# Optimization experiments

Measured on AMD Instinct MI355X. Metric: run time of the kernel, lower is better.

The kernel has to match this reference:

```python
import math
import jax, jax.numpy as jnp
import numpy as np

D_MODEL = 256
N_HEADS = 8
D_K = D_MODEL // N_HEADS
BS = 2
SEQ = 2048
NEG = -1e32


def _linear(x, W, b):
    return x @ W + b


def _layernorm(x, g, b):
    m = jnp.mean(x, axis=-1, keepdims=True)
    v = jnp.mean((x - m) ** 2, axis=-1, keepdims=True)
    return (x - m) / jnp.sqrt(v + 1e-5) * g + b


def _attention(q, k, v, mask, gammas):
    # q,k,v: [b,h,s,dk]; mask: [1,1,s,s] bool; gammas: [h,1,1]
    d_k = q.shape[-1]
    scores = jnp.einsum('bhqd,bhkd->bhqk', q, k) / math.sqrt(d_k)
    S = scores.shape[-1]
    # distance-decay bias (computed under stop_gradient, as torch.no_grad + detach)
    sm = jax.lax.stop_gradient(jax.nn.softmax(jnp.where(mask, scores, NEG), axis=-1))
    distcum = jnp.cumsum(sm, axis=-1)
    disttot = jnp.sum(sm, axis=-1, keepdims=True)
    idx = jnp.arange(S, dtype=scores.dtype)
    pos = jnp.abs(idx[None, :] - idx[:, None])[None, None]  # |i-j|
    dist = jax.lax.stop_gradient(
        jnp.sqrt(jnp.clip((disttot - distcum) * pos, 0.0, None)))
    gamma = -jax.nn.softplus(gammas)[None]  # [1,h,1,1]
    eff = jnp.clip(jnp.exp(dist * gamma), 1e-5, 1e5)
    scores = jnp.where(mask, scores * eff, NEG)
    scores = jnp.where(mask, jax.nn.softmax(scores, axis=-1), 0.0)
    return jnp.einsum('bhqk,bhkd->bhqd', scores, v)


def _mha(qx, kx, vx, Wq, bq, Wk, bk, Wv, bv, Wo, bo, gammas, mask):
    bs = qx.shape[0]
    def split(x, W, b):
        return _linear(x, W, b).reshape(bs, -1, N_HEADS, D_K).transpose(0, 2, 1, 3)
    q = split(qx, Wq, bq)
    k = split(kx, Wk, bk)
    v = split(vx, Wv, bv)
    o = _attention(q, k, v, mask, gammas)
    o = o.transpose(0, 2, 1, 3).reshape(bs, -1, D_MODEL)
    return _linear(o, Wo, bo)


def _layer(query, key, values, Wq, bq, Wk, bk, Wv, bv, Wo, bo, gammas, ln_g, ln_b, peek_cur):
    S = query.shape[1]
    mask = jnp.tril(jnp.ones((S, S), dtype=bool), 0 if peek_cur else -1)[None, None]
    out = _mha(query, key, values, Wq, bq, Wk, bk, Wv, bv, Wo, bo, gammas, mask)
    return _layernorm(query + out, ln_g, ln_b)


def _forward(q_emb, qa_emb,
             b1_Wq, b1_bq, b1_Wv, b1_bv, b1_Wo, b1_bo, b1_gam, b1_lng, b1_lnb,
             b2_Wq, b2_bq, b2_Wv, b2_bv, b2_Wo, b2_bo, b2_gam, b2_lng, b2_lnb,
             b3_Wq, b3_bq, b3_Wk, b3_bk, b3_Wv, b3_bv, b3_Wo, b3_bo, b3_gam, b3_lng, b3_lnb,
             know_params, lk_W, lk_b, lv_W, lv_b):
    # blocks 1 & 2: kq_same -> k projection shares q projection weights
    hq = _layer(q_emb, q_emb, q_emb,
                b1_Wq, b1_bq, b1_Wq, b1_bq, b1_Wv, b1_bv, b1_Wo, b1_bo,
                b1_gam, b1_lng, b1_lnb, peek_cur=True)
    ha = _layer(qa_emb, qa_emb, qa_emb,
                b2_Wq, b2_bq, b2_Wq, b2_bq, b2_Wv, b2_bv, b2_Wo, b2_bo,
                b2_gam, b2_lng, b2_lnb, peek_cur=True)
    query = jnp.broadcast_to(know_params, hq.shape)
    h = _layer(query, hq, ha,
               b3_Wq, b3_bq, b3_Wk, b3_bk, b3_Wv, b3_bv, b3_Wo, b3_bo,
               b3_gam, b3_lng, b3_lnb, peek_cur=False)
    bs, S, d = hq.shape
    key = jax.nn.sigmoid(_linear(
        jnp.broadcast_to(know_params, (bs, S, d)).reshape(bs, S, N_HEADS, D_K),
        lk_W, lk_b)).reshape(bs * S, N_HEADS, d)
    value = jax.nn.sigmoid(_linear(
        h.reshape(bs, S, N_HEADS, D_K), lv_W, lv_b)).reshape(bs * S, N_HEADS, d)
    beta = jnp.einsum('nhd,nd->nh', key, q_emb.reshape(bs * S, d))
    alpha = jax.nn.softmax(beta, axis=-1)
    h = jnp.einsum('nh,nhd->nd', alpha, value).reshape(bs, S, d)
    return h


def setup_inputs() -> dict:
    keys = iter(jax.random.split(jax.random.key(0), 64))
    def nrm(shape, scale=0.02):
        return jax.random.normal(next(keys), shape, dtype=jnp.float32) * scale
    def uni(shape):
        return jax.random.uniform(next(keys), shape, dtype=jnp.float32, minval=-1.0, maxval=1.0)
    d = D_MODEL
    inp = {
        'q_emb': nrm((BS, SEQ, d), 1.0),
        'qa_emb': nrm((BS, SEQ, d), 1.0),
    }
    for blk in ('b1', 'b2'):
        inp[blk + '_Wq'] = nrm((d, d)); inp[blk + '_bq'] = jnp.zeros((d,), jnp.float32)
        inp[blk + '_Wv'] = nrm((d, d)); inp[blk + '_bv'] = jnp.zeros((d,), jnp.float32)
        inp[blk + '_Wo'] = nrm((d, d)); inp[blk + '_bo'] = jnp.zeros((d,), jnp.float32)
        inp[blk + '_gam'] = uni((N_HEADS, 1, 1))
        inp[blk + '_lng'] = jnp.ones((d,), jnp.float32)
        inp[blk + '_lnb'] = jnp.zeros((d,), jnp.float32)
    inp['b3_Wq'] = nrm((d, d)); inp['b3_bq'] = jnp.zeros((d,), jnp.float32)
    inp['b3_Wk'] = nrm((d, d)); inp['b3_bk'] = jnp.zeros((d,), jnp.float32)
    inp['b3_Wv'] = nrm((d, d)); inp['b3_bv'] = jnp.zeros((d,), jnp.float32)
    inp['b3_Wo'] = nrm((d, d)); inp['b3_bo'] = jnp.zeros((d,), jnp.float32)
    inp['b3_gam'] = uni((N_HEADS, 1, 1))
    inp['b3_lng'] = jnp.ones((d,), jnp.float32)
    inp['b3_lnb'] = jnp.zeros((d,), jnp.float32)
    inp['know_params'] = uni((1, 1, d))
    inp['lk_W'] = nrm((D_K, d)); inp['lk_b'] = jnp.zeros((d,), jnp.float32)
    inp['lv_W'] = nrm((D_K, d)); inp['lv_b'] = jnp.zeros((d,), jnp.float32)
    return inp


def reference(q_emb, qa_emb,
              b1_Wq, b1_bq, b1_Wv, b1_bv, b1_Wo, b1_bo, b1_gam, b1_lng, b1_lnb,
              b2_Wq, b2_bq, b2_Wv, b2_bv, b2_Wo, b2_bo, b2_gam, b2_lng, b2_lnb,
              b3_Wq, b3_bq, b3_Wk, b3_bk, b3_Wv, b3_bv, b3_Wo, b3_bo, b3_gam, b3_lng, b3_lnb,
              know_params, lk_W, lk_b, lv_W, lv_b):
    return _forward(q_emb, qa_emb,
                    b1_Wq, b1_bq, b1_Wv, b1_bv, b1_Wo, b1_bo, b1_gam, b1_lng, b1_lnb,
                    b2_Wq, b2_bq, b2_Wv, b2_bv, b2_Wo, b2_bo, b2_gam, b2_lng, b2_lnb,
                    b3_Wq, b3_bq, b3_Wk, b3_bk, b3_Wv, b3_bv, b3_Wo, b3_bo, b3_gam, b3_lng, b3_lnb,
                    know_params, lk_W, lk_b, lv_W, lv_b)
```

## Files before the change

kernel.cpp:

```cpp
#include <hip/hip_runtime.h>
#include <hip/hip_bf16.h>

#define DM 256
#define NH 8
#define DK 32
#define BSZ 2
#define SEQ 2048
#define ROWS (BSZ*SEQ)
#define RT 16
#define SRB 2312

static __device__ __forceinline__ int sw8(int j) { return j + ((j >> 6) << 3); }

typedef __attribute__((ext_vector_type(8))) short short8;
typedef __attribute__((ext_vector_type(4))) float f32x4;

static __device__ __forceinline__ unsigned short f2bf(float f) {
    unsigned u = __float_as_uint(f);
    return (unsigned short)((u + 0x7FFFu + ((u >> 16) & 1u)) >> 16);
}
static __device__ __forceinline__ float bf2f(unsigned short h) {
    return __uint_as_float(((unsigned)h) << 16);
}

static __device__ __forceinline__ unsigned cvtpk(float lo, float hi) {
    unsigned r;
    asm("v_cvt_pk_bf16_f32 %0, %1, %2" : "=v"(r) : "v"(lo), "v"(hi));
    return r;
}

static __device__ __forceinline__ float ex2(float x) { return __builtin_amdgcn_exp2f(x); }
static __device__ __forceinline__ float sqt(float x) { return __builtin_amdgcn_sqrtf(x); }
static __device__ __forceinline__ float rcp(float x) { return __builtin_amdgcn_rcpf(x); }

template<int CTRL, int RM>
static __device__ __forceinline__ float dppadd(float x) {
    int s = __builtin_amdgcn_update_dpp(0, __float_as_int(x), CTRL, RM, 0xf, true);
    return x + __int_as_float(s);
}
static __device__ __forceinline__ float scan32(float x) {
    x = dppadd<0x111, 0xf>(x);
    x = dppadd<0x112, 0xf>(x);
    x = dppadd<0x114, 0xf>(x);
    x = dppadd<0x118, 0xf>(x);
    x = dppadd<0x142, 0xa>(x);
    return x;
}
static __device__ __forceinline__ float red16(float x) {
    x = dppadd<0x0B1, 0xf>(x);
    x = dppadd<0x04E, 0xf>(x);
    x = dppadd<0x124, 0xf>(x);
    x = dppadd<0x128, 0xf>(x);
    return x;
}
static __device__ __forceinline__ float bcast31(float x) {
    return __int_as_float(__builtin_amdgcn_ds_swizzle(__float_as_int(x), 0x03E0));
}
static __device__ __forceinline__ float swz_x16(float x) {
    return __int_as_float(__builtin_amdgcn_ds_swizzle(__float_as_int(x), 0x401F));
}

static __device__ __forceinline__ void unpack4(uint2 u, float& s0, float& s1,
                                               float& s2, float& s3) {
    s0 = __uint_as_float(u.x << 16);
    s1 = __uint_as_float(u.x & 0xFFFF0000u);
    s2 = __uint_as_float(u.y << 16);
    s3 = __uint_as_float(u.y & 0xFFFF0000u);
}

static __device__ __forceinline__ uint2 decay_quad(
    float s0, float s1, float s2, float s3v,
    float e0, float e1, float e2, float e3,
    float cum, float pq, float linv,
    float l, float gamma2, float& l2)
{
    float p0, p1, p2, p3;
    cum += e0;
    { float dist = sqt(fmaxf((l - cum) * pq, 0.f));
      float eff = fmaxf(ex2(dist * gamma2), 1e-5f);
      p0 = ex2(s0 * eff); l2 += p0; }
    cum += e1;
    { float dist = sqt(fmaxf((l - cum) * (pq - linv), 0.f));
      float eff = fmaxf(ex2(dist * gamma2), 1e-5f);
      p1 = ex2(s1 * eff); l2 += p1; }
    cum += e2;
    { float dist = sqt(fmaxf((l - cum) * (pq - 2.f * linv), 0.f));
      float eff = fmaxf(ex2(dist * gamma2), 1e-5f);
      p2 = ex2(s2 * eff); l2 += p2; }
    cum += e3;
    { float dist = sqt(fmaxf((l - cum) * (pq - 3.f * linv), 0.f));
      float eff = fmaxf(ex2(dist * gamma2), 1e-5f);
      p3 = ex2(s3v * eff); l2 += p3; }
    uint2 st;
    st.x = cvtpk(p0, p1);
    st.y = cvtpk(p2, p3);
    return st;
}

#define MFMA_BF16 __builtin_amdgcn_mfma_f32_16x16x32_bf16
#define LOG2E 1.44269504088896340736f

static __device__ __forceinline__ float waveRedSum(float v) {
    #pragma unroll
    for (int off = 32; off > 0; off >>= 1) v += __shfl_down(v, off, 64);
    return v;
}

__global__ __launch_bounds__(256) void convert_w_kernel(
    const float* __restrict__ S0, const float* __restrict__ S1, const float* __restrict__ S2,
    const float* __restrict__ S3, const float* __restrict__ S4, const float* __restrict__ S5,
    const float* __restrict__ S6, const float* __restrict__ S7, const float* __restrict__ S8,
    unsigned short* __restrict__ dst,
    const float* __restrict__ know,
    const float* __restrict__ W3q, const float* __restrict__ b3q,
    const float* __restrict__ lkW, const float* __restrict__ lkb,
    float* __restrict__ q3row, float* __restrict__ key8)
{
    __shared__ float kn[DM];
    int s = blockIdx.y;
    if (s == 9) {
        if (blockIdx.x != 0) return;
        int t = threadIdx.x;
        kn[t] = know[t];
        __syncthreads();
        float acc = b3q[t];
        for (int c = 0; c < DM; ++c) acc += kn[c] * W3q[(size_t)c * DM + t];
        q3row[t] = acc;
        float bk = lkb[t];
        for (int h = 0; h < NH; ++h) {
            float a = bk;
            #pragma unroll
            for (int c = 0; c < DK; ++c) a += kn[h * DK + c] * lkW[(size_t)c * DM + t];
            key8[(size_t)h * DM + t] = 1.f / (1.f + __expf(-a));
        }
        return;
    }
    const float* W;
    if (s == 0) W = S0; else if (s == 1) W = S1; else if (s == 2) W = S2;
    else if (s == 3) W = S3; else if (s == 4) W = S4; else if (s == 5) W = S5;
    else if (s == 6) W = S6; else if (s == 7) W = S7; else W = S8;
    unsigned short* H = dst + (size_t)s * 131072;
    unsigned short* L = H + 65536;

    int e = blockIdx.x * 1024 + threadIdx.x * 4;
    int k = e >> 8, n = e & 255;
    float4 w4 = *(const float4*)(W + e);
    float v[4] = {w4.x, w4.y, w4.z, w4.w};
    #pragma unroll
    for (int i = 0; i < 4; ++i) {
        unsigned short h = f2bf(v[i]);
        H[(size_t)(n + i) * 256 + k] = h;
        L[(size_t)(n + i) * 256 + k] = (unsigned short)f2bf(v[i] - bf2f(h));
    }
}

__global__ __launch_bounds__(256) void gemm4_kernel(
    const float* __restrict__ X0, const unsigned short* __restrict__ H0, const float* __restrict__ B0,
    float* __restrict__ Y0, unsigned short* __restrict__ K0o, unsigned short* __restrict__ V0o,
    const float* __restrict__ X1, const unsigned short* __restrict__ H1, const float* __restrict__ B1,
    float* __restrict__ Y1, unsigned short* __restrict__ K1o, unsigned short* __restrict__ V1o,
    const float* __restrict__ X2, const unsigned short* __restrict__ H2, const float* __restrict__ B2,
    float* __restrict__ Y2, unsigned short* __restrict__ K2o, unsigned short* __restrict__ V2o,
    const float* __restrict__ X3, const unsigned short* __restrict__ H3, const float* __restrict__ B3,
    float* __restrict__ Y3, unsigned short* __restrict__ K3o, unsigned short* __restrict__ V3o)
{
    const float *X, *Bias; const unsigned short* H; float* Yf;
    unsigned short *KSo, *VSo;
    int s = blockIdx.y;
    if (s == 0)      { X = X0; H = H0; Bias = B0; Yf = Y0; KSo = K0o; VSo = V0o; }
    else if (s == 1) { X = X1; H = H1; Bias = B1; Yf = Y1; KSo = K1o; VSo = V1o; }
    else if (s == 2) { X = X2; H = H2; Bias = B2; Yf = Y2; KSo = K2o; VSo = V2o; }
    else             { X = X3; H = H3; Bias = B3; Yf = Y3; KSo = K3o; VSo = V3o; }
    const unsigned short* L = H + 65536;

    __shared__ __align__(16) unsigned short XhL[16 * 264];
    __shared__ __align__(16) unsigned short XlL[16 * 264];
    __shared__ __align__(16) unsigned short vt[256][24];
    int t = threadIdx.x;
    int r0 = blockIdx.x * 16;
    {
        int r = t >> 4, c0 = (t & 15) * 16;
        const float* xp = X + (size_t)(r0 + r) * DM + c0;
        #pragma unroll
        for (int i = 0; i < 16; i += 4) {
            float4 v4 = *(const float4*)(xp + i);
            float vv[4] = {v4.x, v4.y, v4.z, v4.w};
            #pragma unroll
            for (int j = 0; j < 4; ++j) {
                unsigned short h = f2bf(vv[j]);
                XhL[r * 264 + c0 + i + j] = h;
                XlL[r * 264 + c0 + i + j] = (unsigned short)f2bf(vv[j] - bf2f(h));
            }
        }
    }
    __syncthreads();
    int lane = t & 63, wv = t >> 6;
    int m = lane & 15, quad = lane >> 4;
    f32x4 aa[4];
    #pragma unroll
    for (int nt = 0; nt < 4; ++nt) { aa[nt][0]=0.f; aa[nt][1]=0.f; aa[nt][2]=0.f; aa[nt][3]=0.f; }
    #pragma unroll 1
    for (int kc = 0; kc < 8; ++kc) {
        int k0 = kc * 32;
        short8 Ah = *(const short8*)&XhL[m * 264 + k0 + quad * 8];
        short8 Al = *(const short8*)&XlL[m * 264 + k0 + quad * 8];
        size_t boff = (size_t)(wv * 64 + m) * 256 + k0 + quad * 8;
        #pragma unroll
        for (int nt = 0; nt < 4; ++nt) {
            short8 Bh = *(const short8*)(H + boff + nt * 16 * 256);
            short8 Bl = *(const short8*)(L + boff + nt * 16 * 256);
            aa[nt] = MFMA_BF16(Al, Bh, aa[nt], 0, 0, 0);
            aa[nt] = MFMA_BF16(Ah, Bl, aa[nt], 0, 0, 0);
            aa[nt] = MFMA_BF16(Ah, Bh, aa[nt], 0, 0, 0);
        }
    }
    int col0 = wv * 64 + m;
    #pragma unroll
    for (int nt = 0; nt < 4; ++nt) {
        int col = col0 + nt * 16;
        float bb = Bias[col];
        float yv[4];
        #pragma unroll
        for (int g = 0; g < 4; ++g) yv[g] = aa[nt][g] + bb;
        if (Yf) {
            #pragma unroll
            for (int g = 0; g < 4; ++g)
                Yf[(size_t)(r0 + quad * 4 + g) * DM + col] = yv[g];
        }
        if (KSo) {
            unsigned short* KH = KSo;
            unsigned short* KL = KSo + (size_t)ROWS * DM;
            #pragma unroll
            for (int g = 0; g < 4; ++g) {
                unsigned short hb = f2bf(yv[g]);
                KH[(size_t)(r0 + quad * 4 + g) * DM + col] = hb;
                KL[(size_t)(r0 + quad * 4 + g) * DM + col] =
                    (unsigned short)f2bf(yv[g] - bf2f(hb));
            }
        }
        if (VSo) {
            ushort4 h4;
            h4.x = f2bf(yv[0]); h4.y = f2bf(yv[1]);
            h4.z = f2bf(yv[2]); h4.w = f2bf(yv[3]);
            *(ushort4*)&vt[col][quad * 4] = h4;
        }
    }
    if (VSo) {
        __syncthreads();
        short8 v0 = *(const short8*)&vt[t][0];
        short8 v1 = *(const short8*)&vt[t][8];
        unsigned short* vp = VSo + (size_t)t * ROWS + r0;
        *(short8*)vp = v0;
        *(short8*)(vp + 8) = v1;
    }
}

__global__ __launch_bounds__(256) void gemm_ln2_kernel(
    const float* __restrict__ X0, const unsigned short* __restrict__ H0, const float* __restrict__ B0,
    const float* __restrict__ R0, const float* __restrict__ G0, const float* __restrict__ L0,
    float* __restrict__ Y0, int bc0,
    const float* __restrict__ X1, const unsigned short* __restrict__ H1, const float* __restrict__ B1,
    const float* __restrict__ R1, const float* __restrict__ G1, const float* __restrict__ L1,
    float* __restrict__ Y1, int bc1)
{
    const float *X, *Bias, *R, *G, *Lb; const unsigned short* H; float* Y; int bc;
    if (blockIdx.y == 0) { X=X0; H=H0; Bias=B0; R=R0; G=G0; Lb=L0; Y=Y0; bc=bc0; }
    else                 { X=X1; H=H1; Bias=B1; R=R1; G=G1; Lb=L1; Y=Y1; bc=bc1; }
    const unsigned short* L = H + 65536;

    __shared__ __align__(16) unsigned short XhL[16 * 264];
    __shared__ __align__(16) unsigned short XlL[16 * 264];
    __shared__ __align__(16) float yl[16 * 260];
    int t = threadIdx.x;
    int r0 = blockIdx.x * 16;
    {   int r = t >> 4, c0 = (t & 15) * 16;
        const float* xp = X + (size_t)(r0 + r) * DM + c0;
        #pragma unroll
        for (int i = 0; i < 16; i += 4) {
            float4 v4 = *(const float4*)(xp + i);
            float vv[4] = {v4.x, v4.y, v4.z, v4.w};
            #pragma unroll
            for (int j = 0; j < 4; ++j) {
                unsigned short h = f2bf(vv[j]);
                XhL[r * 264 + c0 + i + j] = h;
                XlL[r * 264 + c0 + i + j] = (unsigned short)f2bf(vv[j] - bf2f(h));
            }
        }
    }
    __syncthreads();
    int lane = t & 63, wv = t >> 6;
    int m = lane & 15, quad = lane >> 4;
    f32x4 aa[4];
    #pragma unroll
    for (int nt = 0; nt < 4; ++nt) { aa[nt][0]=0.f; aa[nt][1]=0.f; aa[nt][2]=0.f; aa[nt][3]=0.f; }
    #pragma unroll 1
    for (int kc = 0; kc < 8; ++kc) {
        int k0 = kc * 32;
        short8 Ah = *(const short8*)&XhL[m * 264 + k0 + quad * 8];
        short8 Al = *(const short8*)&XlL[m * 264 + k0 + quad * 8];
        size_t boff = (size_t)(wv * 64 + m) * 256 + k0 + quad * 8;
        #pragma unroll
        for (int nt = 0; nt < 4; ++nt) {
            short8 Bh = *(const short8*)(H + boff + nt * 16 * 256);
            short8 Bl = *(const short8*)(L + boff + nt * 16 * 256);
            aa[nt] = MFMA_BF16(Al, Bh, aa[nt], 0, 0, 0);
            aa[nt] = MFMA_BF16(Ah, Bl, aa[nt], 0, 0, 0);
            aa[nt] = MFMA_BF16(Ah, Bh, aa[nt], 0, 0, 0);
        }
    }
    {
        int col0 = wv * 64 + m;
        #pragma unroll
        for (int nt = 0; nt < 4; ++nt) {
            int col = col0 + nt * 16;
            float bb = Bias[col];
            #pragma unroll
            for (int g = 0; g < 4; ++g) {
                int row = quad * 4 + g;
                float res = bc ? R[col] : R[(size_t)(r0 + row) * DM + col];
                yl[row * 260 + col] = aa[nt][g] + bb + res;
            }
        }
    }
    __syncthreads();
    {
        int r = t >> 4, c0 = (t & 15) * 16;
        float vals[16];
        float part = 0.f;
        #pragma unroll
        for (int i = 0; i < 16; ++i) { vals[i] = yl[r * 260 + c0 + i]; part += vals[i]; }
        #pragma unroll
        for (int off = 8; off; off >>= 1) part += __shfl_xor(part, off, 16);
        float mean = part * (1.f / DM);
        float vp = 0.f;
        #pragma unroll
        for (int i = 0; i < 16; ++i) { float d = vals[i] - mean; vp += d * d; }
        #pragma unroll
        for (int off = 8; off; off >>= 1) vp += __shfl_xor(vp, off, 16);
        float rs = rsqrtf(vp * (1.f / DM) + 1e-5f);
        float* yp = Y + (size_t)(r0 + r) * DM + c0;
        #pragma unroll
        for (int i = 0; i < 16; i += 4) {
            float4 o;
            o.x = (vals[i+0] - mean) * rs * G[c0+i+0] + Lb[c0+i+0];
            o.y = (vals[i+1] - mean) * rs * G[c0+i+1] + Lb[c0+i+1];
            o.z = (vals[i+2] - mean) * rs * G[c0+i+2] + Lb[c0+i+2];
            o.w = (vals[i+3] - mean) * rs * G[c0+i+3] + Lb[c0+i+3];
            *(float4*)(yp + i) = o;
        }
    }
}

__global__ __launch_bounds__(256) void score3a_kernel(
    const float* __restrict__ q3row, const float* __restrict__ K3,
    unsigned short* __restrict__ S3, float* __restrict__ C3,
    float* __restrict__ Csum)
{
    __shared__ float wsum[4];
    int s = blockIdx.x;
    int bh = blockIdx.y;
    int b = bh >> 3, h = bh & 7;
    int t = threadIdx.x;
    int lane = t & 63, wv = t >> 6;
    int j = s * 256 + t;
    const float scaleL2 = 0.17677669529663687f * LOG2E;
    float qv[DK];
    #pragma unroll
    for (int d = 0; d < DK; d += 4) {
        float4 qq = *(const float4*)(q3row + h * DK + d);
        qv[d+0] = qq.x * scaleL2; qv[d+1] = qq.y * scaleL2;
        qv[d+2] = qq.z * scaleL2; qv[d+3] = qq.w * scaleL2;
    }
    const float* kp = K3 + ((size_t)b * SEQ + j) * DM + h * DK;
    float kv[DK];
    #pragma unroll
    for (int d = 0; d < DK; d += 4) {
        float4 kq = *(const float4*)(kp + d);
        kv[d+0] = kq.x; kv[d+1] = kq.y; kv[d+2] = kq.z; kv[d+3] = kq.w;
    }
    float sc = 0.f;
    #pragma unroll
    for (int d = 0; d < DK; ++d) sc += qv[d] * kv[d];
    unsigned short sb16 = f2bf(sc);
    float e = ex2(bf2f(sb16));
    float x = e;
    #pragma unroll
    for (int off = 1; off < 64; off <<= 1) {
        float y = __shfl_up(x, off, 64);
        if (lane >= off) x += y;
    }
    if (lane == 63) wsum[wv] = x;
    __syncthreads();
    float woff = 0.f;
    for (int w = 0; w < wv; ++w) woff += wsum[w];
    float inc = woff + x;
    S3[(size_t)bh * SEQ + j] = sb16;
    C3[(size_t)bh * SEQ + j] = inc;
    if (t == 255) Csum[bh * 8 + s] = inc;
}

__global__ __launch_bounds__(256) void score3b_kernel(
    const float* __restrict__ Csum, float* __restrict__ C3)
{
    int s = blockIdx.x + 1;
    int bh = blockIdx.y;
    int t = threadIdx.x;
    float off = 0.f;
    for (int w = 0; w < s; ++w) off += Csum[bh * 8 + w];
    C3[(size_t)bh * SEQ + s * 256 + t] += off;
}

__global__ __launch_bounds__(512) void attn_tile_kernel(
    const float* __restrict__ Q0,
    const unsigned short* __restrict__ KS0, const unsigned short* __restrict__ VS0,
    const float* __restrict__ g0, float* __restrict__ O0,
    const float* __restrict__ Q1,
    const unsigned short* __restrict__ KS1, const unsigned short* __restrict__ VS1,
    const float* __restrict__ g1, float* __restrict__ O1,
    const unsigned short* __restrict__ S3g, const float* __restrict__ C3g,
    int peek, int qbcast)
{
    __shared__ __align__(16) unsigned short SB[RT * SRB];
    __shared__ float qs[RT][DK];
    __shared__ float l2inv_s[RT];
    __shared__ float rowsum[8 * RT];

    int bx, by;
    {
        int flat = (int)blockIdx.y * 128 + (int)blockIdx.x;
        int per = ((int)gridDim.y * 128) >> 3;
        int nf = (flat & 7) * per + (flat >> 3);
        by = nf >> 7;
        bx = nf & 127;
    }
    int y = by;
    int set = y >> 4, bh = y & 15;
    const float* Q = set ? Q1 : Q0;
    const unsigned short* KS = set ? KS1 : KS0;
    const unsigned short* VS = set ? VS1 : VS0;
    const float* gm = set ? g1 : g0;
    float* O = set ? O1 : O0;

    int b = bh >> 3, h = bh & 7;
    int i0 = (127 - bx) * RT;
    int t = threadIdx.x;
    size_t base = ((size_t)b * SEQ) * DM + (size_t)h * DK;

    int njAll = peek ? (i0 + RT) : (i0 + RT - 1);
    int njPad32 = (njAll + 31) & ~31;
    int njPad128 = (njAll + 127) & ~127;
    const float scaleL2 = 0.17677669529663687f * LOG2E;

    if (!qbcast) {
        {
            int r = t >> 5, d = t & 31;
            qs[r][d] = Q[base + (size_t)(i0 + r) * DM + d];
        }
        __syncthreads();

        {
            int wave = t >> 6, lane = t & 63;
            int m = lane & 15, quad = lane >> 4;

            float av[8];
            {
                float4 qa = *(const float4*)&qs[m][8 * quad];
                float4 qb = *(const float4*)&qs[m][8 * quad + 4];
                av[0]=qa.x*scaleL2; av[1]=qa.y*scaleL2; av[2]=qa.z*scaleL2; av[3]=qa.w*scaleL2;
                av[4]=qb.x*scaleL2; av[5]=qb.y*scaleL2; av[6]=qb.z*scaleL2; av[7]=qb.w*scaleL2;
            }
            short8 Ah;
            #pragma unroll
            for (int i = 0; i < 8; ++i) Ah[i] = (short)f2bf(av[i]);

            const unsigned short* KH = KS;
            const unsigned short* KL = KS + (size_t)ROWS * DM;
            size_t rowb = (size_t)b * SEQ;
            int njr0 = i0 + quad * 4 + peek;
            float rp0 = 0.f, rp1 = 0.f, rp2 = 0.f, rp3 = 0.f;
            int nChunks = (njAll + 15) >> 4;
            #pragma unroll 2
            for (int c = wave; c < nChunks; c += 8) {
                int j0 = c << 4;
                size_t off = (rowb + j0 + m) * DM + h * DK + quad * 8;
                short8 Bh = *(const short8*)&KH[off];
                short8 Bl = *(const short8*)&KL[off];
                f32x4 acc = {0.f, 0.f, 0.f, 0.f};
                acc = MFMA_BF16(Ah, Bl, acc, 0, 0, 0);
                acc = MFMA_BF16(Ah, Bh, acc, 0, 0, 0);
                int jcol = j0 + m;
                int sj = sw8(jcol);
                unsigned pk01 = cvtpk(acc[0], acc[1]);
                unsigned pk23 = cvtpk(acc[2], acc[3]);
                SB[(quad * 4 + 0) * SRB + sj] = (unsigned short)pk01;
                SB[(quad * 4 + 1) * SRB + sj] = (unsigned short)(pk01 >> 16);
                SB[(quad * 4 + 2) * SRB + sj] = (unsigned short)pk23;
                SB[(quad * 4 + 3) * SRB + sj] = (unsigned short)(pk23 >> 16);
                rp0 += (jcol < njr0 + 0) ? ex2(acc[0]) : 0.f;
                rp1 += (jcol < njr0 + 1) ? ex2(acc[1]) : 0.f;
                rp2 += (jcol < njr0 + 2) ? ex2(acc[2]) : 0.f;
                rp3 += (jcol < njr0 + 3) ? ex2(acc[3]) : 0.f;
            }
            rp0 = red16(rp0); rp1 = red16(rp1);
            rp2 = red16(rp2); rp3 = red16(rp3);
            if (m == 0) {
                rowsum[wave * RT + quad * 4 + 0] = rp0;
                rowsum[wave * RT + quad * 4 + 1] = rp1;
                rowsum[wave * RT + quad * 4 + 2] = rp2;
                rowsum[wave * RT + quad * 4 + 3] = rp3;
            }
        }
        __syncthreads();

        {
            int r = t >> 5, c = t & 31;
            int i = i0 + r;
            int nj = peek ? (i + 1) : i;
            for (int j = nj + c; j < njPad128; j += 32)
                SB[r * SRB + sw8(j)] = 0xFF80u;
        }
        __syncthreads();
    }

    if (qbcast) {
        int r = t >> 5, c = t & 31;
        int i = i0 + r;
        int nj = peek ? (i + 1) : i;
        unsigned short* Sr = SB + r * SRB;
        float gamma2 = -log1pf(__expf(gm[h])) * LOG2E;
        const unsigned short* s3p = S3g + (size_t)bh * SEQ;
        const float* c3p = C3g + (size_t)bh * SEQ;
        float Lc = (nj > 0) ? c3p[nj - 1] : 0.f;
        float linv = (nj > 0) ? rcp(Lc) : 0.f;
        float li2 = linv + linv, li3 = li2 + linv;
        float l2 = 0.f;
        int nIt = (njPad32 + 127) >> 7;
        int j4 = 4 * c;
        uint2 su_a = *(const uint2*)&s3p[j4];
        float4 C4_a = *(const float4*)&c3p[j4];
        int jp = (j4 + 128 < SEQ - 3) ? j4 + 128 : SEQ - 4;
        uint2 su_b = *(const uint2*)&s3p[jp];
        float4 C4_b = *(const float4*)&c3p[jp];
        #pragma unroll 1
        for (int k = 0; k < nIt; ++k, j4 += 128) {
            uint2 su = su_a; float4 C4 = C4_a;
            su_a = su_b; C4_a = C4_b;
            int jn = (j4 + 256 < SEQ - 3) ? j4 + 256 : SEQ - 4;
            su_b = *(const uint2*)&s3p[jn];
            C4_b = *(const float4*)&c3p[jn];
            float s0 = __uint_as_float(su.x << 16);
            float s1 = __uint_as_float(su.x & 0xFFFF0000u);
            float s2 = __uint_as_float(su.y << 16);
            float s3v = __uint_as_float(su.y & 0xFFFF0000u);
            float pq = (float)(i - j4) * linv;
            float p0, p1, p2, p3;
            { float dist = sqt(fmaxf((Lc - C4.x) * pq, 0.f));
              float eff = fmaxf(ex2(dist * gamma2), 1e-5f);
              p0 = (j4 + 0 < nj) ? ex2(s0 * eff) : 0.f; l2 += p0; }
            { float dist = sqt(fmaxf((Lc - C4.y) * (pq - linv), 0.f));
              float eff = fmaxf(ex2(dist * gamma2), 1e-5f);
              p1 = (j4 + 1 < nj) ? ex2(s1 * eff) : 0.f; l2 += p1; }
            { float dist = sqt(fmaxf((Lc - C4.z) * (pq - li2), 0.f));
              float eff = fmaxf(ex2(dist * gamma2), 1e-5f);
              p2 = (j4 + 2 < nj) ? ex2(s2 * eff) : 0.f; l2 += p2; }
            { float dist = sqt(fmaxf((Lc - C4.w) * (pq - li3), 0.f));
              float eff = fmaxf(ex2(dist * gamma2), 1e-5f);
              p3 = (j4 + 3 < nj) ? ex2(s3v * eff) : 0.f; l2 += p3; }
            uint2 st;
            st.x = cvtpk(p0, p1);
            st.y = cvtpk(p2, p3);
            *(uint2*)&Sr[sw8(j4)] = st;
        }
        l2 = red16(l2);
        l2 += swz_x16(l2);
        if (c == 0) l2inv_s[r] = (nj > 0) ? rcp(l2) : 0.f;
    } else {
        int r = t >> 5, c = t & 31;
        int i = i0 + r;
        int nj = peek ? (i + 1) : i;
        unsigned short* Sr = SB + r * SRB;
        float gamma2 = -log1pf(__expf(gm[h])) * LOG2E;

        float l = 0.f;
        #pragma unroll
        for (int w = 0; w < 8; ++w) l += rowsum[w * RT + r];
        float linv = rcp(l);

        float l2 = 0.f;
        float Bc = 0.f;
        int nIter = (njPad32 + 127) >> 7;
        int pairs = nIter >> 1;
        uint2 nxA, nxB;
        nxA = *(const uint2*)&Sr[sw8(4 * c)];
        nxB = *(const uint2*)&Sr[sw8(4 * c + 128)];
        #pragma unroll 1
        for (int k = 0; k < pairs; ++k) {
            int j4a = 256 * k + 4 * c;
            int j4b = j4a + 128;
            uint2 uA = nxA;
            uint2 uB = nxB;
            nxA = *(const uint2*)&Sr[sw8(j4a + 256)];
            nxB = *(const uint2*)&Sr[sw8(j4b + 256)];
            float a0, a1, a2, a3, b0, b1, b2, b3;
            unpack4(uA, a0, a1, a2, a3);
            unpack4(uB, b0, b1, b2, b3);
            float eA0 = ex2(a0), eA1 = ex2(a1), eA2 = ex2(a2), eA3 = ex2(a3);
            float eB0 = ex2(b0), eB1 = ex2(b1), eB2 = ex2(b2), eB3 = ex2(b3);
            float sigA = eA0 + eA1 + eA2 + eA3;
            float sigB = eB0 + eB1 + eB2 + eB3;
            float xA = scan32(sigA);
            float xB = scan32(sigB);
            float totA = bcast31(xA);
            float totB = bcast31(xB);
            float cumA = Bc + (xA - sigA);
            float cumB = Bc + totA + (xB - sigB);
            Bc += totA + totB;
            float pqA = (float)(i - j4a) * linv;
            float pqB = pqA - 128.f * linv;
            uint2 stA = decay_quad(a0, a1, a2, a3, eA0, eA1, eA2, eA3,
                                   cumA, pqA, linv, l, gamma2, l2);
            uint2 stB = decay_quad(b0, b1, b2, b3, eB0, eB1, eB2, eB3,
                                   cumB, pqB, linv, l, gamma2, l2);
            *(uint2*)&Sr[sw8(j4a)] = stA;
            *(uint2*)&Sr[sw8(j4b)] = stB;
        }
        if (nIter & 1) {
            int j4a = 256 * pairs + 4 * c;
            uint2 uA = nxA;
            float a0, a1, a2, a3;
            unpack4(uA, a0, a1, a2, a3);
            float eA0 = ex2(a0), eA1 = ex2(a1), eA2 = ex2(a2), eA3 = ex2(a3);
            float sigA = eA0 + eA1 + eA2 + eA3;
            float xA = scan32(sigA);
            float cumA = Bc + (xA - sigA);
            float pqA = (float)(i - j4a) * linv;
            uint2 stA = decay_quad(a0, a1, a2, a3, eA0, eA1, eA2, eA3,
                                   cumA, pqA, linv, l, gamma2, l2);
            *(uint2*)&Sr[sw8(j4a)] = stA;
        }
        l2 = red16(l2);
        l2 += swz_x16(l2);
        if (c == 0) l2inv_s[r] = (nj > 0) ? rcp(l2) : 0.f;
    }
    __syncthreads();

    {
        int wave = t >> 6, lane = t & 63;
        int n16 = lane & 15, quad = lane >> 4;
        const unsigned short* VH = VS;
        size_t vb0 = (size_t)(h * DK + n16) * ROWS + (size_t)b * SEQ;
        size_t vb1 = (size_t)(h * DK + 16 + n16) * ROWS + (size_t)b * SEQ;
        f32x4 oc0 = {0.f,0.f,0.f,0.f}, oc1 = {0.f,0.f,0.f,0.f};
        #pragma unroll 2
        for (int j0 = wave * 32; j0 < njPad32; j0 += 256) {
            short8 Ap = *(const short8*)&SB[n16 * SRB + sw8(j0 + quad * 8)];
            int jo = j0 + quad * 8;
            short8 Bh0 = *(const short8*)&VH[vb0 + jo];
            short8 Bh1 = *(const short8*)&VH[vb1 + jo];
            oc0 = MFMA_BF16(Ap, Bh0, oc0, 0, 0, 0);
            oc1 = MFMA_BF16(Ap, Bh1, oc1, 0, 0, 0);
        }
        __syncthreads();
        float* FS = (float*)SB;
        {
            #pragma unroll
            for (int g = 0; g < 4; ++g) {
                int row = quad * 4 + g;
                FS[wave * 512 + row * 32 + n16] = oc0[g];
                FS[wave * 512 + row * 32 + 16 + n16] = oc1[g];
            }
        }
    }
    __syncthreads();
    {
        float* FS = (float*)SB;
        int r2 = t >> 5, d = t & 31;
        float sum = 0.f;
        #pragma unroll
        for (int w = 0; w < 8; ++w)
            sum += FS[w * 512 + r2 * 32 + d];
        int ii = i0 + r2;
        O[base + (size_t)ii * DM + d] = sum * l2inv_s[r2];
    }
}

__global__ __launch_bounds__(256) void readout_kernel(
    const float* __restrict__ h3, const float* __restrict__ qe,
    const float* __restrict__ key8,
    const float* __restrict__ lvW, const float* __restrict__ lvb,
    float* __restrict__ out)
{
    __shared__ float hrow[DM], qrow[DM];
    __shared__ float red8[4][NH];
    int n = blockIdx.x, t = threadIdx.x;
    int lane = t & 63, wid = t >> 6;
    hrow[t] = h3[(size_t)n * DM + t];
    qrow[t] = qe[(size_t)n * DM + t];
    __syncthreads();
    float ph[NH];
    #pragma unroll
    for (int h = 0; h < NH; ++h) {
        float v = key8[(size_t)h * DM + t] * qrow[t];
        v = waveRedSum(v);
        ph[h] = v;
    }
    if (lane == 0) {
        #pragma unroll
        for (int h = 0; h < NH; ++h) red8[wid][h] = ph[h];
    }
    __syncthreads();
    float beta[NH];
    #pragma unroll
    for (int h = 0; h < NH; ++h)
        beta[h] = red8[0][h] + red8[1][h] + red8[2][h] + red8[3][h];
    float bv = lvb[t];
    float vh[NH];
    for (int h = 0; h < NH; ++h) {
        float a = bv;
        #pragma unroll
        for (int c = 0; c < DK; ++c) a += hrow[h * DK + c] * lvW[(size_t)c * DM + t];
        vh[h] = 1.f / (1.f + __expf(-a));
    }
    float mb = beta[0];
    #pragma unroll
    for (int h = 1; h < NH; ++h) mb = fmaxf(mb, beta[h]);
    float se = 0.f, eh[NH];
    #pragma unroll
    for (int h = 0; h < NH; ++h) { eh[h] = __expf(beta[h] - mb); se += eh[h]; }
    float sinv = 1.f / se;
    float o = 0.f;
    #pragma unroll
    for (int h = 0; h < NH; ++h) o += eh[h] * sinv * vh[h];
    out[(size_t)n * DM + t] = o;
}

extern "C" void kernel_launch(void* const* d_in, const int* in_sizes, int n_in,
                              void* d_out, int out_size, void* d_ws, size_t ws_size,
                              hipStream_t stream) {
    (void)in_sizes; (void)n_in; (void)out_size; (void)ws_size;
    const float* q_emb  = (const float*)d_in[0];
    const float* qa_emb = (const float*)d_in[1];
    const float* b1_Wq = (const float*)d_in[2];
    const float* b1_bq = (const float*)d_in[3];
    const float* b1_Wv = (const float*)d_in[4];
    const float* b1_bv = (const float*)d_in[5];
    const float* b1_Wo = (const float*)d_in[6];
    const float* b1_bo = (const float*)d_in[7];
    const float* b1_gam = (const float*)d_in[8];
    const float* b1_lng = (const float*)d_in[9];
    const float* b1_lnb = (const float*)d_in[10];
    const float* b2_Wq = (const float*)d_in[11];
    const float* b2_bq = (const float*)d_in[12];
    const float* b2_Wv = (const float*)d_in[13];
    const float* b2_bv = (const float*)d_in[14];
    const float* b2_Wo = (const float*)d_in[15];
    const float* b2_bo = (const float*)d_in[16];
    const float* b2_gam = (const float*)d_in[17];
    const float* b2_lng = (const float*)d_in[18];
    const float* b2_lnb = (const float*)d_in[19];
    const float* b3_Wq = (const float*)d_in[20];
    const float* b3_bq = (const float*)d_in[21];
    const float* b3_Wk = (const float*)d_in[22];
    const float* b3_bk = (const float*)d_in[23];
    const float* b3_Wv = (const float*)d_in[24];
    const float* b3_bv = (const float*)d_in[25];
    const float* b3_Wo = (const float*)d_in[26];
    const float* b3_bo = (const float*)d_in[27];
    const float* b3_gam = (const float*)d_in[28];
    const float* b3_lng = (const float*)d_in[29];
    const float* b3_lnb = (const float*)d_in[30];
    const float* know  = (const float*)d_in[31];
    const float* lk_W  = (const float*)d_in[32];
    const float* lk_b  = (const float*)d_in[33];
    const float* lv_W  = (const float*)d_in[34];
    const float* lv_b  = (const float*)d_in[35];

    const size_t SLAB = (size_t)ROWS * DM;
    const size_t USLAB = 2 * SLAB;
    float* A1 = (float*)d_ws;
    float* A2 = A1 + SLAB;
    float* C1 = A2 + SLAB;
    float* C2 = C1 + SLAB;
    unsigned short* KS1 = (unsigned short*)(C2 + SLAB);
    unsigned short* KS2 = KS1 + USLAB;
    unsigned short* VS1 = KS2 + USLAB;
    unsigned short* VS2 = VS1 + USLAB;
    float* q3row = (float*)(VS2 + USLAB);
    float* key8  = q3row + DM;
    unsigned short* Wsp = (unsigned short*)(key8 + NH * DM);
    unsigned short* S3buf = Wsp + (size_t)9 * 131072;
    float* C3buf = (float*)(S3buf + 16 * SEQ);
    float* Csum  = C3buf + 16 * SEQ;
    float* hq = (float*)KS1;
    float* ha = (float*)KS2;
    float* k3 = A1;
    unsigned short* VS3 = VS1;
    float* O3 = C1;
    float* h3 = C2;

    auto WH = [&](int i) { return Wsp + (size_t)i * 131072; };

    dim3 blk(256);
    dim3 ablk(512);
    dim3 agrid2(SEQ / RT, 32);
    dim3 agrid1(SEQ / RT, 16);
    dim3 rgrid(ROWS);

    convert_w_kernel<<<dim3(64, 10), blk, 0, stream>>>(
        b1_Wq, b1_Wv, b1_Wo, b2_Wq, b2_Wv, b2_Wo, b3_Wk, b3_Wv, b3_Wo, Wsp,
        know, b3_Wq, b3_bq, lk_W, lk_b, q3row, key8);

    gemm4_kernel<<<dim3(ROWS/16, 4), blk, 0, stream>>>(
        q_emb,  WH(0), b1_bq, A1,      KS1,     nullptr,
        q_emb,  WH(1), b1_bv, nullptr, nullptr, VS1,
        qa_emb, WH(3), b2_bq, A2,      KS2,     nullptr,
        qa_emb, WH(4), b2_bv, nullptr, nullptr, VS2);

    attn_tile_kernel<<<agrid2, ablk, 0, stream>>>(
        A1, KS1, VS1, b1_gam, C1,
        A2, KS2, VS2, b2_gam, C2,
        nullptr, nullptr, 1, 0);

    gemm_ln2_kernel<<<dim3(ROWS/16, 2), blk, 0, stream>>>(
        C1, WH(2), b1_bo, q_emb,  b1_lng, b1_lnb, hq, 0,
        C2, WH(5), b2_bo, qa_emb, b2_lng, b2_lnb, ha, 0);

    gemm4_kernel<<<dim3(ROWS/16, 2), blk, 0, stream>>>(
        hq, WH(6), b3_bk, k3,      nullptr, nullptr,
        ha, WH(7), b3_bv, nullptr, nullptr, VS3,
        hq, WH(6), b3_bk, k3,      nullptr, nullptr,
        hq, WH(6), b3_bk, k3,      nullptr, nullptr);

    score3a_kernel<<<dim3(8, 16), blk, 0, stream>>>(q3row, k3, S3buf, C3buf, Csum);
    score3b_kernel<<<dim3(7, 16), blk, 0, stream>>>(Csum, C3buf);

    attn_tile_kernel<<<agrid1, ablk, 0, stream>>>(
        q3row, nullptr, VS3, b3_gam, O3,
        q3row, nullptr, VS3, b3_gam, O3,
        S3buf, C3buf, 0, 1);

    gemm_ln2_kernel<<<dim3(ROWS/16, 1), blk, 0, stream>>>(
        O3, WH(8), b3_bo, know, b3_lng, b3_lnb, h3, 1,
        O3, WH(8), b3_bo, know, b3_lng, b3_lnb, h3, 1);

    readout_kernel<<<rgrid, blk, 0, stream>>>(h3, q_emb, key8, lv_W, lv_b,
                                              (float*)d_out);
}
```

Baseline: 420.1 us.

## Split attention kernel into specialized block1/2 and block3 variants with chunked LDS

```diff
diff --git a/kernel.cpp b/kernel.cpp
--- a/kernel.cpp
+++ b/kernel.cpp
@@ -9,6 +9,7 @@
 #define ROWS (BSZ*SEQ)
 #define RT 16
 #define SRB 2312
+#define SRBH 1144
 
 static __device__ __forceinline__ int sw8(int j) { return j + ((j >> 6) << 3); }
 
@@ -410,15 +411,13 @@
     C3[(size_t)bh * SEQ + s * 256 + t] += off;
 }
 
-__global__ __launch_bounds__(512) void attn_tile_kernel(
+__global__ __launch_bounds__(512) void attn12_kernel(
     const float* __restrict__ Q0,
     const unsigned short* __restrict__ KS0, const unsigned short* __restrict__ VS0,
     const float* __restrict__ g0, float* __restrict__ O0,
     const float* __restrict__ Q1,
     const unsigned short* __restrict__ KS1, const unsigned short* __restrict__ VS1,
-    const float* __restrict__ g1, float* __restrict__ O1,
-    const unsigned short* __restrict__ S3g, const float* __restrict__ C3g,
-    int peek, int qbcast)
+    const float* __restrict__ g1, float* __restrict__ O1)
 {
     __shared__ __align__(16) unsigned short SB[RT * SRB];
     __shared__ float qs[RT][DK];
@@ -428,13 +427,12 @@
     int bx, by;
     {
         int flat = (int)blockIdx.y * 128 + (int)blockIdx.x;
-        int per = ((int)gridDim.y * 128) >> 3;
+        int per = (32 * 128) >> 3;
         int nf = (flat & 7) * per + (flat >> 3);
         by = nf >> 7;
         bx = nf & 127;
     }
-    int y = by;
-    int set = y >> 4, bh = y & 15;
+    int set = by >> 4, bh = by & 15;
     const float* Q = set ? Q1 : Q0;
     const unsigned short* KS = set ? KS1 : KS0;
     const unsigned short* VS = set ? VS1 : VS0;
@@ -446,138 +444,82 @@
     int t = threadIdx.x;
     size_t base = ((size_t)b * SEQ) * DM + (size_t)h * DK;
 
-    int njAll = peek ? (i0 + RT) : (i0 + RT - 1);
+    int njAll = i0 + RT;
     int njPad32 = (njAll + 31) & ~31;
     int njPad128 = (njAll + 127) & ~127;
     const float scaleL2 = 0.17677669529663687f * LOG2E;
 
-    if (!qbcast) {
+    {
+        int r = t >> 5, d = t & 31;
+        qs[r][d] = Q[base + (size_t)(i0 + r) * DM + d];
+    }
+    __syncthreads();
+
+    {
+        int wave = t >> 6, lane = t & 63;
+        int m = lane & 15, quad = lane >> 4;
+
+        float av[8];
         {
-            int r = t >> 5, d = t & 31;
-            qs[r][d] = Q[base + (size_t)(i0 + r) * DM + d];
-        }
-        __syncthreads();
-
-        {
-            int wave = t >> 6, lane = t & 63;
-            int m = lane & 15, quad = lane >> 4;
-
-            float av[8];
-            {
-                float4 qa = *(const float4*)&qs[m][8 * quad];
-                float4 qb = *(const float4*)&qs[m][8 * quad + 4];
-                av[0]=qa.x*scaleL2; av[1]=qa.y*scaleL2; av[2]=qa.z*scaleL2; av[3]=qa.w*scaleL2;
-                av[4]=qb.x*scaleL2; av[5]=qb.y*scaleL2; av[6]=qb.z*scaleL2; av[7]=qb.w*scaleL2;
-            }
-            short8 Ah;
-            #pragma unroll
-            for (int i = 0; i < 8; ++i) Ah[i] = (short)f2bf(av[i]);
-
-            const unsigned short* KH = KS;
-            const unsigned short* KL = KS + (size_t)ROWS * DM;
-            size_t rowb = (size_t)b * SEQ;
-            int njr0 = i0 + quad * 4 + peek;
-            float rp0 = 0.f, rp1 = 0.f, rp2 = 0.f, rp3 = 0.f;
-            int nChunks = (njAll + 15) >> 4;
-            #pragma unroll 2
-            for (int c = wave; c < nChunks; c += 8) {
-                int j0 = c << 4;
-                size_t off = (rowb + j0 + m) * DM + h * DK + quad * 8;
-                short8 Bh = *(const short8*)&KH[off];
-                short8 Bl = *(const short8*)&KL[off];
-                f32x4 acc = {0.f, 0.f, 0.f, 0.f};
-                acc = MFMA_BF16(Ah, Bl, acc, 0, 0, 0);
-                acc = MFMA_BF16(Ah, Bh, acc, 0, 0, 0);
-                int jcol = j0 + m;
-                int sj = sw8(jcol);
-                unsigned pk01 = cvtpk(acc[0], acc[1]);
-                unsigned pk23 = cvtpk(acc[2], acc[3]);
-                SB[(quad * 4 + 0) * SRB + sj] = (unsigned short)pk01;
-                SB[(quad * 4 + 1) * SRB + sj] = (unsigned short)(pk01 >> 16);
-                SB[(quad * 4 + 2) * SRB + sj] = (unsigned short)pk23;
-                SB[(quad * 4 + 3) * SRB + sj] = (unsigned short)(pk23 >> 16);
-                rp0 += (jcol < njr0 + 0) ? ex2(acc[0]) : 0.f;
-                rp1 += (jcol < njr0 + 1) ? ex2(acc[1]) : 0.f;
-                rp2 += (jcol < njr0 + 2) ? ex2(acc[2]) : 0.f;
-                rp3 += (jcol < njr0 + 3) ? ex2(acc[3]) : 0.f;
-            }
-            rp0 = red16(rp0); rp1 = red16(rp1);
-            rp2 = red16(rp2); rp3 = red16(rp3);
-            if (m == 0) {
-                rowsum[wave * RT + quad * 4 + 0] = rp0;
-                rowsum[wave * RT + quad * 4 + 1] = rp1;
-                rowsum[wave * RT + quad * 4 + 2] = rp2;
-                rowsum[wave * RT + quad * 4 + 3] = rp3;
-            }
-        }
-        __syncthreads();
-
-        {
-            int r = t >> 5, c = t & 31;
-            int i = i0 + r;
-            int nj = peek ? (i + 1) : i;
-            for (int j = nj + c; j < njPad128; j += 32)
-                SB[r * SRB + sw8(j)] = 0xFF80u;
-        }
-        __syncthreads();
-    }
-
-    if (qbcast) {
+            float4 qa = *(const float4*)&qs[m][8 * quad];
+            float4 qb = *(const float4*)&qs[m][8 * quad + 4];
+            av[0]=qa.x*scaleL2; av[1]=qa.y*scaleL2; av[2]=qa.z*scaleL2; av[3]=qa.w*scaleL2;
+            av[4]=qb.x*scaleL2; av[5]=qb.y*scaleL2; av[6]=qb.z*scaleL2; av[7]=qb.w*scaleL2;
+        }
+        short8 Ah;
+        #pragma unroll
+        for (int i = 0; i < 8; ++i) Ah[i] = (short)f2bf(av[i]);
+
+        const unsigned short* KH = KS;
+        const unsigned short* KL = KS + (size_t)ROWS * DM;
+        size_t rowb = (size_t)b * SEQ;
+        int njr0 = i0 + quad * 4 + 1;
+        float rp0 = 0.f, rp1 = 0.f, rp2 = 0.f, rp3 = 0.f;
+        int nChunks = (njAll + 15) >> 4;
+        #pragma unroll 2
+        for (int c = wave; c < nChunks; c += 8) {
+            int j0 = c << 4;
+            size_t off = (rowb + j0 + m) * DM + h * DK + quad * 8;
+            short8 Bh = *(const short8*)&KH[off];
+            short8 Bl = *(const short8*)&KL[off];
+            f32x4 acc = {0.f, 0.f, 0.f, 0.f};
+            acc = MFMA_BF16(Ah, Bl, acc, 0, 0, 0);
+            acc = MFMA_BF16(Ah, Bh, acc, 0, 0, 0);
+            int jcol = j0 + m;
+            int sj = sw8(jcol);
+            unsigned pk01 = cvtpk(acc[0], acc[1]);
+            unsigned pk23 = cvtpk(acc[2], acc[3]);
+            SB[(quad * 4 + 0) * SRB + sj] = (unsigned short)pk01;
+            SB[(quad * 4 + 1) * SRB + sj] = (unsigned short)(pk01 >> 16);
+            SB[(quad * 4 + 2) * SRB + sj] = (unsigned short)pk23;
+            SB[(quad * 4 + 3) * SRB + sj] = (unsigned short)(pk23 >> 16);
+            rp0 += (jcol < njr0 + 0) ? ex2(acc[0]) : 0.f;
+            rp1 += (jcol < njr0 + 1) ? ex2(acc[1]) : 0.f;
+            rp2 += (jcol < njr0 + 2) ? ex2(acc[2]) : 0.f;
+            rp3 += (jcol < njr0 + 3) ? ex2(acc[3]) : 0.f;
+        }
+        rp0 = red16(rp0); rp1 = red16(rp1);
+        rp2 = red16(rp2); rp3 = red16(rp3);
+        if (m == 0) {
+            rowsum[wave * RT + quad * 4 + 0] = rp0;
+            rowsum[wave * RT + quad * 4 + 1] = rp1;
+            rowsum[wave * RT + quad * 4 + 2] = rp2;
+            rowsum[wave * RT + quad * 4 + 3] = rp3;
+        }
+    }
+    __syncthreads();
+
+    {
+        int r = t >> 5, c = t & 31;
+        int nj = i0 + r + 1;
+        for (int j = nj + c; j < njPad128; j += 32)
+            SB[r * SRB + sw8(j)] = 0xFF80u;
+    }
+    __syncthreads();
+
+    {
         int r = t >> 5, c = t & 31;
         int i = i0 + r;
-        int nj = peek ? (i + 1) : i;
-        unsigned short* Sr = SB + r * SRB;
-        float gamma2 = -log1pf(__expf(gm[h])) * LOG2E;
-        const unsigned short* s3p = S3g + (size_t)bh * SEQ;
-        const float* c3p = C3g + (size_t)bh * SEQ;
-        float Lc = (nj > 0) ? c3p[nj - 1] : 0.f;
-        float linv = (nj > 0) ? rcp(Lc) : 0.f;
-        float li2 = linv + linv, li3 = li2 + linv;
-        float l2 = 0.f;
-        int nIt = (njPad32 + 127) >> 7;
-        int j4 = 4 * c;
-        uint2 su_a = *(const uint2*)&s3p[j4];
-        float4 C4_a = *(const float4*)&c3p[j4];
-        int jp = (j4 + 128 < SEQ - 3) ? j4 + 128 : SEQ - 4;
-        uint2 su_b = *(const uint2*)&s3p[jp];
-        float4 C4_b = *(const float4*)&c3p[jp];
-        #pragma unroll 1
-        for (int k = 0; k < nIt; ++k, j4 += 128) {
-            uint2 su = su_a; float4 C4 = C4_a;
-            su_a = su_b; C4_a = C4_b;
-            int jn = (j4 + 256 < SEQ - 3) ? j4 + 256 : SEQ - 4;
-            su_b = *(const uint2*)&s3p[jn];
-            C4_b = *(const float4*)&c3p[jn];
-            float s0 = __uint_as_float(su.x << 16);
-            float s1 = __uint_as_float(su.x & 0xFFFF0000u);
-            float s2 = __uint_as_float(su.y << 16);
-            float s3v = __uint_as_float(su.y & 0xFFFF0000u);
-            float pq = (float)(i - j4) * linv;
-            float p0, p1, p2, p3;
-            { float dist = sqt(fmaxf((Lc - C4.x) * pq, 0.f));
-              float eff = fmaxf(ex2(dist * gamma2), 1e-5f);
-              p0 = (j4 + 0 < nj) ? ex2(s0 * eff) : 0.f; l2 += p0; }
-            { float dist = sqt(fmaxf((Lc - C4.y) * (pq - linv), 0.f));
-              float eff = fmaxf(ex2(dist * gamma2), 1e-5f);
-              p1 = (j4 + 1 < nj) ? ex2(s1 * eff) : 0.f; l2 += p1; }
-            { float dist = sqt(fmaxf((Lc - C4.z) * (pq - li2), 0.f));
-              float eff = fmaxf(ex2(dist * gamma2), 1e-5f);
-              p2 = (j4 + 2 < nj) ? ex2(s2 * eff) : 0.f; l2 += p2; }
-            { float dist = sqt(fmaxf((Lc - C4.w) * (pq - li3), 0.f));
-              float eff = fmaxf(ex2(dist * gamma2), 1e-5f);
-              p3 = (j4 + 3 < nj) ? ex2(s3v * eff) : 0.f; l2 += p3; }
-            uint2 st;
-            st.x = cvtpk(p0, p1);
-            st.y = cvtpk(p2, p3);
-            *(uint2*)&Sr[sw8(j4)] = st;
-        }
-        l2 = red16(l2);
-        l2 += swz_x16(l2);
-        if (c == 0) l2inv_s[r] = (nj > 0) ? rcp(l2) : 0.f;
-    } else {
-        int r = t >> 5, c = t & 31;
-        int i = i0 + r;
-        int nj = peek ? (i + 1) : i;
         unsigned short* Sr = SB + r * SRB;
         float gamma2 = -log1pf(__expf(gm[h])) * LOG2E;
 
@@ -640,7 +582,7 @@
         }
         l2 = red16(l2);
         l2 += swz_x16(l2);
-        if (c == 0) l2inv_s[r] = (nj > 0) ? rcp(l2) : 0.f;
+        if (c == 0) l2inv_s[r] = rcp(l2);
     }
     __syncthreads();
 
@@ -662,13 +604,11 @@
         }
         __syncthreads();
         float* FS = (float*)SB;
-        {
-            #pragma unroll
-            for (int g = 0; g < 4; ++g) {
-                int row = quad * 4 + g;
-                FS[wave * 512 + row * 32 + n16] = oc0[g];
-                FS[wave * 512 + row * 32 + 16 + n16] = oc1[g];
-            }
+        #pragma unroll
+        for (int g = 0; g < 4; ++g) {
+            int row = quad * 4 + g;
+            FS[wave * 512 + row * 32 + n16] = oc0[g];
+            FS[wave * 512 + row * 32 + 16 + n16] = oc1[g];
         }
     }
     __syncthreads();
@@ -679,8 +619,117 @@
         #pragma unroll
         for (int w = 0; w < 8; ++w)
             sum += FS[w * 512 + r2 * 32 + d];
-        int ii = i0 + r2;
-        O[base + (size_t)ii * DM + d] = sum * l2inv_s[r2];
+        O[base + (size_t)(i0 + r2) * DM + d] = sum * l2inv_s[r2];
+    }
+}
+
+__global__ __launch_bounds__(512) void attn3_kernel(
+    const unsigned short* __restrict__ VS, const float* __restrict__ gm8,
+    float* __restrict__ O,
+    const unsigned short* __restrict__ S3g, const float* __restrict__ C3g)
+{
+    __shared__ __align__(16) unsigned short SBH[RT * SRBH];
+    __shared__ float l2inv_s[RT];
+
+    int bx, by;
+    {
+        int flat = (int)blockIdx.y * 128 + (int)blockIdx.x;
+        int per = (16 * 128) >> 3;
+        int nf = (flat & 7) * per + (flat >> 3);
+        by = nf >> 7;
+        bx = nf & 127;
+    }
+    int bh = by;
+    int b = bh >> 3, h = bh & 7;
+    int i0 = (127 - bx) * RT;
+    int t = threadIdx.x;
+    size_t base = ((size_t)b * SEQ) * DM + (size_t)h * DK;
+
+    int njAll = i0 + RT - 1;
+    int njPad32 = (njAll + 31) & ~31;
+    int E = ((njPad32 + 127) >> 7) << 7;
+
+    int r = t >> 5, c = t & 31;
+    int i = i0 + r;
+    int nj = i;
+    unsigned short* Sr = SBH + r * SRBH;
+    float gamma2 = -log1pf(__expf(gm8[h])) * LOG2E;
+    const unsigned short* s3p = S3g + (size_t)bh * SEQ;
+    const float* c3p = C3g + (size_t)bh * SEQ;
+    float Lc = (nj > 0) ? c3p[nj - 1] : 0.f;
+    float linv = (nj > 0) ? rcp(Lc) : 0.f;
+    float li2 = linv + linv, li3 = li2 + linv;
+    float l2 = 0.f;
+
+    int wave = t >> 6, lane = t & 63;
+    int n16 = lane & 15, quad = lane >> 4;
+    size_t rowb = (size_t)b * SEQ;
+    size_t vb0 = (size_t)(h * DK + n16) * ROWS + rowb;
+    size_t vb1 = (size_t)(h * DK + 16 + n16) * ROWS + rowb;
+    f32x4 oc0 = {0.f,0.f,0.f,0.f}, oc1 = {0.f,0.f,0.f,0.f};
+
+    #pragma unroll 1
+    for (int hbase = 0; hbase < E; hbase += 1024) {
+        int hend = min(hbase + 1024, E);
+        #pragma unroll 1
+        for (int j4 = hbase + 4 * c; j4 < hend; j4 += 128) {
+            uint2 su = *(const uint2*)&s3p[j4];
+            float4 C4 = *(const float4*)&c3p[j4];
+            float s0 = __uint_as_float(su.x << 16);
+            float s1 = __uint_as_float(su.x & 0xFFFF0000u);
+            float s2 = __uint_as_float(su.y << 16);
+            float s3v = __uint_as_float(su.y & 0xFFFF0000u);
+            float pq = (float)(i - j4) * linv;
+            float p0, p1, p2, p3;
+            { float dist = sqt(fmaxf((Lc - C4.x) * pq, 0.f));
+              float eff = fmaxf(ex2(dist * gamma2), 1e-5f);
+              p0 = (j4 + 0 < nj) ? ex2(s0 * eff) : 0.f; l2 += p0; }
+            { float dist = sqt(fmaxf((Lc - C4.y) * (pq - linv), 0.f));
+              float eff = fmaxf(ex2(dist * gamma2), 1e-5f);
+              p1 = (j4 + 1 < nj) ? ex2(s1 * eff) : 0.f; l2 += p1; }
+            { float dist = sqt(fmaxf((Lc - C4.z) * (pq - li2), 0.f));
+              float eff = fmaxf(ex2(dist * gamma2), 1e-5f);
+              p2 = (j4 + 2 < nj) ? ex2(s2 * eff) : 0.f; l2 += p2; }
+            { float dist = sqt(fmaxf((Lc - C4.w) * (pq - li3), 0.f));
+              float eff = fmaxf(ex2(dist * gamma2), 1e-5f);
+              p3 = (j4 + 3 < nj) ? ex2(s3v * eff) : 0.f; l2 += p3; }
+            uint2 st;
+            st.x = cvtpk(p0, p1);
+            st.y = cvtpk(p2, p3);
+            *(uint2*)&Sr[sw8(j4 - hbase)] = st;
+        }
+        __syncthreads();
+        int pend = min(hbase + 1024, njPad32);
+        #pragma unroll 1
+        for (int j0 = hbase + wave * 32; j0 < pend; j0 += 256) {
+            short8 Ap = *(const short8*)&SBH[n16 * SRBH + sw8(j0 - hbase + quad * 8)];
+            int jo = j0 + quad * 8;
+            short8 Bh0 = *(const short8*)&VS[vb0 + jo];
+            short8 Bh1 = *(const short8*)&VS[vb1 + jo];
+            oc0 = MFMA_BF16(Ap, Bh0, oc0, 0, 0, 0);
+            oc1 = MFMA_BF16(Ap, Bh1, oc1, 0, 0, 0);
+        }
+        __syncthreads();
+    }
+
+    l2 = red16(l2);
+    l2 += swz_x16(l2);
+    if (c == 0) l2inv_s[r] = (nj > 0) ? rcp(l2) : 0.f;
+    float* FS = (float*)SBH;
+    #pragma unroll
+    for (int g = 0; g < 4; ++g) {
+        int row = quad * 4 + g;
+        FS[wave * 512 + row * 32 + n16] = oc0[g];
+        FS[wave * 512 + row * 32 + 16 + n16] = oc1[g];
+    }
+    __syncthreads();
+    {
+        int r2 = t >> 5, d = t & 31;
+        float sum = 0.f;
+        #pragma unroll
+        for (int w = 0; w < 8; ++w)
+            sum += FS[w * 512 + r2 * 32 + d];
+        O[base + (size_t)(i0 + r2) * DM + d] = sum * l2inv_s[r2];
     }
 }
 
@@ -816,10 +865,9 @@
         qa_emb, WH(3), b2_bq, A2,      KS2,     nullptr,
         qa_emb, WH(4), b2_bv, nullptr, nullptr, VS2);
 
-    attn_tile_kernel<<<agrid2, ablk, 0, stream>>>(
+    attn12_kernel<<<agrid2, ablk, 0, stream>>>(
         A1, KS1, VS1, b1_gam, C1,
-        A2, KS2, VS2, b2_gam, C2,
-        nullptr, nullptr, 1, 0);
+        A2, KS2, VS2, b2_gam, C2);
 
     gemm_ln2_kernel<<<dim3(ROWS/16, 2), blk, 0, stream>>>(
         C1, WH(2), b1_bo, q_emb,  b1_lng, b1_lnb, hq, 0,
@@ -834,10 +882,7 @@
     score3a_kernel<<<dim3(8, 16), blk, 0, stream>>>(q3row, k3, S3buf, C3buf, Csum);
     score3b_kernel<<<dim3(7, 16), blk, 0, stream>>>(Csum, C3buf);
 
-    attn_tile_kernel<<<agrid1, ablk, 0, stream>>>(
-        q3row, nullptr, VS3, b3_gam, O3,
-        q3row, nullptr, VS3, b3_gam, O3,
-        S3buf, C3buf, 0, 1);
+    attn3_kernel<<<agrid1, ablk, 0, stream>>>(VS3, b3_gam, O3, S3buf, C3buf);
 
     gemm_ln2_kernel<<<dim3(ROWS/16, 1), blk, 0, stream>>>(
         O3, WH(8), b3_bo, know, b3_lng, b3_lnb, h3, 1,
```

Result: no change. 425.3 us (+1.2%).
